# Performance work log

Measured on AMD Instinct MI355X. Metric: run time of the kernel, lower is better.

Reference implementation:

```python
import jax, jax.numpy as jnp
import numpy as np

K_F = 3          # propagation kernel
PAD_F = 1
NUM = K_F * K_F - 1   # 8 non-reference neighbors
IDX_REF = NUM // 2    # 4
PROP_TIME = 18
B, H, W = 4, 240, 1216


def _conv2d_same(x, w, b):
    # x: (B,Cin,H,W), w: (Cout,Cin,kh,kw)
    y = jax.lax.conv_general_dilated(x, w, (1, 1), 'SAME',
                                     dimension_numbers=('NCHW', 'OIHW', 'NCHW'))
    return y + b[None, :, None, None]


def _bilinear(img, y, x):
    # img: (B,H,W); y,x: (B,K,H,W) float sample coords. Zero outside bounds (DCN semantics).
    Bv, Hv, Wv = img.shape
    flat = img.reshape(Bv, -1)
    y0 = jnp.floor(y)
    x0 = jnp.floor(x)
    wy = y - y0
    wx = x - x0

    def g(yy, xx):
        valid = (yy >= 0) & (yy <= Hv - 1) & (xx >= 0) & (xx <= Wv - 1)
        yc = jnp.clip(yy, 0, Hv - 1).astype(jnp.int32)
        xc = jnp.clip(xx, 0, Wv - 1).astype(jnp.int32)
        idx = (yc * Wv + xc).reshape(Bv, -1)
        v = jnp.take_along_axis(flat, idx, axis=1).reshape(yy.shape)
        return jnp.where(valid, v, jnp.zeros((), img.dtype))

    return ((1 - wy) * (1 - wx) * g(y0, x0)
            + (1 - wy) * wx * g(y0, x0 + 1)
            + wy * (1 - wx) * g(y1 := y0 + 1, x0)
            + wy * wx * g(y1, x0 + 1))


def _deform_agg(feat, off, mask, k, pad):
    # Modulated deformable conv with w == 1, b == 0, ch_f == 1.
    # feat: (B,1,H,W); off: (B,K,2,H,W) (dy,dx); mask: (B,K,H,W)
    Bv, _, Hv, Wv = feat.shape
    kk = jnp.arange(k)
    by = (jnp.repeat(kk, k) - pad).astype(feat.dtype)  # kernel base dy, row-major
    bx = (jnp.tile(kk, k) - pad).astype(feat.dtype)    # kernel base dx
    gy = jnp.arange(Hv, dtype=feat.dtype)[None, None, :, None]
    gx = jnp.arange(Wv, dtype=feat.dtype)[None, None, None, :]
    y = gy + by[None, :, None, None] + off[:, :, 0]
    x = gx + bx[None, :, None, None] + off[:, :, 1]
    s = _bilinear(feat[:, 0], y, x)                    # (B,K,H,W)
    return jnp.sum(s * mask, axis=1, keepdims=True)


def setup_inputs() -> dict:
    key = jax.random.key(0)
    k1, k2, k3, k4, k5, k6 = jax.random.split(key, 6)
    feat_init = jax.random.uniform(k1, (B, 1, H, W), jnp.float32)
    guidance = jax.random.normal(k2, (B, 8, H, W), jnp.float32)
    confidence = jax.random.uniform(k3, (B, 1, H, W), jnp.float32)
    dep = jax.random.uniform(k4, (B, 1, H, W), jnp.float32)
    valid = (jax.random.uniform(k5, (B, 1, H, W), jnp.float32) < 0.05)
    feat_fix = dep * valid.astype(jnp.float32)
    w_oa = 0.1 * jax.random.normal(k6, (3 * NUM, 8, 3, 3), jnp.float32)
    b_oa = jnp.zeros((3 * NUM,), jnp.float32)
    aff_scale_const = jnp.full((1,), 0.5 * NUM, jnp.float32)  # gamma * num (TGASS)
    return {'feat_init': feat_init, 'guidance': guidance, 'confidence': confidence,
            'feat_fix': feat_fix, 'w_oa': w_oa, 'b_oa': b_oa,
            'aff_scale_const': aff_scale_const}


def reference(feat_init, guidance, confidence, feat_fix, w_oa, b_oa, aff_scale_const):
    Bv, _, Hv, Wv = guidance.shape
    oa = _conv2d_same(guidance, w_oa, b_oa)                 # (B,24,H,W)
    o1, o2, aff = oa[:, :NUM], oa[:, NUM:2 * NUM], oa[:, 2 * NUM:]
    # torch: cat((o1,o2),1).view(B,num,2,H,W) then insert zero ref offset at idx_ref
    off = jnp.concatenate([o1, o2], axis=1).reshape(Bv, NUM, 2, Hv, Wv)
    zeros = jnp.zeros((Bv, 1, 2, Hv, Wv), off.dtype)
    off = jnp.concatenate([off[:, :IDX_REF], zeros, off[:, IDX_REF:]], axis=1)  # (B,9,2,H,W)

    # TGASS affinity
    aff = jnp.tanh(aff) / (aff_scale_const + 1e-8)          # (B,8,H,W)

    # confidence-weighted affinity: 1x1 deform-sample of confidence at each neighbor offset
    nbr = jnp.array([0, 1, 2, 3, 5, 6, 7, 8])
    off_c = jax.lax.stop_gradient(off[:, nbr])              # (B,8,2,H,W), offsets detached
    gy = jnp.arange(Hv, dtype=aff.dtype)[None, None, :, None]
    gx = jnp.arange(Wv, dtype=aff.dtype)[None, None, None, :]
    conf_aff = _bilinear(confidence[:, 0], gy + off_c[:, :, 0], gx + off_c[:, :, 1])
    aff = aff * conf_aff

    s = jnp.sum(jnp.abs(aff), axis=1, keepdims=True) + 1e-4
    s = jnp.maximum(s, 1.0)                                 # TGASS clamp
    aff = aff / s
    aff_ref = 1.0 - jnp.sum(aff, axis=1, keepdims=True)
    aff9 = jnp.concatenate([aff[:, :IDX_REF], aff_ref, aff[:, IDX_REF:]], axis=1)  # (B,9,H,W)

    # preserve_input mask
    mask_fix = (jnp.sum((feat_fix > 0.0).astype(feat_fix.dtype), axis=1, keepdims=True) > 0.0)
    mask_fix = jax.lax.stop_gradient(mask_fix.astype(feat_fix.dtype))

    def step(feat, _):
        feat = (1.0 - mask_fix) * feat + mask_fix * feat_fix
        feat = _deform_agg(feat, off, aff9, K_F, PAD_F)
        return feat, None

    feat_result, _ = jax.lax.scan(step, feat_init, None, length=PROP_TIME)
    return feat_result, off.reshape(Bv, -1, Hv, Wv), aff9
```

## Files before the change

kernel.cpp:

```cpp
#include <hip/hip_runtime.h>
#include <hip/hip_bf16.h>

#define B_ 4
#define H_ 240
#define W_ 1216
#define HW_ (H_*W_)
#define N1_ (B_*HW_)
#define PT_ 18

#define PR_ 2
#define TROWS2 (PR_ + 10)
#define TCOLS 274

__device__ __forceinline__ bool probe_bf16(const void* scale_ptr) {
    return ((const unsigned short*)scale_ptr)[0] == 0x4080;
}

__device__ __forceinline__ float ldin(const void* p, int i, bool bf) {
    if (bf) {
        unsigned int u = (unsigned int)((const unsigned short*)p)[i];
        return __uint_as_float(u << 16);
    }
    return ((const float*)p)[i];
}

__device__ __forceinline__ void stout(void* p, int i, bool bf, float v) {
    if (bf) ((__hip_bfloat16*)p)[i] = __float2bfloat16(v);
    else    ((float*)p)[i] = v;
}

template<bool BF>
__device__ __forceinline__ float ldT(const void* p, int i) {
    if (BF) {
        unsigned int u = (unsigned int)((const unsigned short*)p)[i];
        return __uint_as_float(u << 16);
    }
    return ((const float*)p)[i];
}

template<bool BF>
__device__ __forceinline__ void stT(void* p, int i, float v) {
    if (BF) ((__hip_bfloat16*)p)[i] = __float2bfloat16(v);
    else    ((float*)p)[i] = v;
}

__global__ __launch_bounds__(256) void k_prep_w(const void* __restrict__ w_oa,
                                                const void* __restrict__ b_oa,
                                                const void* __restrict__ scale,
                                                float* __restrict__ wc) {
    bool bf = probe_bf16(scale);
    int i = blockIdx.x * 256 + threadIdx.x;
    if (i < 1728) wc[i] = ldin(w_oa, i, bf);
    if (i < 24)   wc[1728 + i] = ldin(b_oa, i, bf);
}

__global__ __launch_bounds__(256) void k_init(const void* __restrict__ finit,
                                              const void* __restrict__ ffix,
                                              const void* __restrict__ scale,
                                              float* __restrict__ featA,
                                              float* __restrict__ featB,
                                              unsigned long long* __restrict__ mask64) {
    bool bf = probe_bf16(scale);
    int p = blockIdx.x * 256 + threadIdx.x;
    float fx = ldin(ffix, p, bf);
    float fi = ldin(finit, p, bf);
    bool fixed = fx > 0.0f;
    float v = fixed ? fx : fi;
    featA[p] = v;
    featB[p] = v;
    unsigned long long bal = __ballot(fixed);
    if ((threadIdx.x & 63) == 0) mask64[p >> 6] = bal;
}

__global__ __launch_bounds__(256) void k_conv(const void* __restrict__ guid,
                                              const void* __restrict__ conf,
                                              const void* __restrict__ scale,
                                              const float* __restrict__ wc,
                                              void* __restrict__ d_out,
                                              float* __restrict__ ws_off,
                                              float* __restrict__ ws_aff,
                                              int mode2) {
    bool bf = probe_bf16(scale);
    int p = blockIdx.x * 256 + threadIdx.x;
    if (p >= N1_) return;
    int b = p / HW_;
    int r = p - b * HW_;
    int h = r / W_;
    int w = r - h * W_;

    float g[8][9];
    #pragma unroll
    for (int t = 0; t < 9; ++t) {
        int hh = h + t / 3 - 1;
        int ww = w + t % 3 - 1;
        bool v = (hh >= 0) && (hh < H_) && (ww >= 0) && (ww < W_);
        int idx0 = hh * W_ + ww;
        #pragma unroll
        for (int ci = 0; ci < 8; ++ci)
            g[ci][t] = v ? ldin(guid, (b * 8 + ci) * HW_ + idx0, bf) : 0.0f;
    }

    float oa[24];
    #pragma unroll
    for (int co = 0; co < 24; ++co) {
        float a = wc[1728 + co];
        #pragma unroll
        for (int ci = 0; ci < 8; ++ci)
            #pragma unroll
            for (int t = 0; t < 9; ++t)
                a = fmaf(g[ci][t], wc[(co * 8 + ci) * 9 + t], a);
        oa[co] = a;
    }

    float scl = ldin(scale, 0, bf);
    float inv = 1.0f / (scl + 1e-8f);

    float aft[8];
    int cbase = b * HW_;
    #pragma unroll
    for (int t = 0; t < 8; ++t) {
        float a = tanhf(oa[16 + t]) * inv;
        float y = (float)h + oa[2 * t];
        float x = (float)w + oa[2 * t + 1];
        float y0f = floorf(y), x0f = floorf(x);
        int y0 = (int)y0f, x0 = (int)x0f;
        float wy = y - y0f, wx = x - x0f;
        int y0c = min(max(y0, 0), H_ - 1), y1c = min(max(y0 + 1, 0), H_ - 1);
        int x0c = min(max(x0, 0), W_ - 1), x1c = min(max(x0 + 1, 0), W_ - 1);
        bool vy0 = (y0 >= 0) && (y0 < H_), vy1 = (y0 >= -1) && (y0 < H_ - 1);
        bool vx0 = (x0 >= 0) && (x0 < W_), vx1 = (x0 >= -1) && (x0 < W_ - 1);
        float w00 = (1.0f - wy) * (1.0f - wx); w00 = (vy0 && vx0) ? w00 : 0.0f;
        float w01 = (1.0f - wy) * wx;          w01 = (vy0 && vx1) ? w01 : 0.0f;
        float w10 = wy * (1.0f - wx);          w10 = (vy1 && vx0) ? w10 : 0.0f;
        float w11 = wy * wx;                   w11 = (vy1 && vx1) ? w11 : 0.0f;
        float f00 = ldin(conf, cbase + y0c * W_ + x0c, bf);
        float f01 = ldin(conf, cbase + y0c * W_ + x1c, bf);
        float f10 = ldin(conf, cbase + y1c * W_ + x0c, bf);
        float f11 = ldin(conf, cbase + y1c * W_ + x1c, bf);
        float cv = w00 * f00 + w01 * f01 + w10 * f10 + w11 * f11;
        aft[t] = a * cv;
    }
    float s = 1e-4f;
    #pragma unroll
    for (int t = 0; t < 8; ++t) s += fabsf(aft[t]);
    s = fmaxf(s, 1.0f);
    float rs = 1.0f / s;
    float suma = 0.0f;
    #pragma unroll
    for (int t = 0; t < 8; ++t) { aft[t] *= rs; suma += aft[t]; }
    float aref = 1.0f - suma;

    #pragma unroll
    for (int t = 0; t < 8; ++t) {
        int n9 = t + (t >= 4 ? 1 : 0);
        stout(d_out, N1_ + (b * 18 + 2 * n9)     * HW_ + r, bf, oa[2 * t]);
        stout(d_out, N1_ + (b * 18 + 2 * n9 + 1) * HW_ + r, bf, oa[2 * t + 1]);
        stout(d_out, 19 * N1_ + (b * 9 + n9) * HW_ + r, bf, aft[t]);
    }
    stout(d_out, N1_ + (b * 18 + 8) * HW_ + r, bf, 0.0f);
    stout(d_out, N1_ + (b * 18 + 9) * HW_ + r, bf, 0.0f);
    stout(d_out, 19 * N1_ + (b * 9 + 4) * HW_ + r, bf, aref);

    if (mode2 && bf) {
        #pragma unroll
        for (int t = 0; t < 8; ++t) {
            ws_off[t * N1_ + p]       = oa[2 * t];
            ws_off[(8 + t) * N1_ + p] = oa[2 * t + 1];
            int n9 = t + (t >= 4 ? 1 : 0);
            ws_aff[n9 * N1_ + p] = aft[t];
        }
        ws_aff[4 * N1_ + p] = aref;
    }
}

template<bool BF>
__device__ __forceinline__ void prop_body(float (*tile)[TCOLS],
                                          const float* __restrict__ src,
                                          float* __restrict__ dst,
                                          const float* __restrict__ ws_off,
                                          const float* __restrict__ ws_aff,
                                          const void* __restrict__ d_out_all,
                                          const unsigned long long* __restrict__ mask64,
                                          void* __restrict__ d_out_feat,
                                          int last, int mode2) {
    int tx = threadIdx.x;
    int bx = blockIdx.x;
    int h0 = blockIdx.y * PR_;
    int b  = blockIdx.z;
    int w  = bx * 256 + tx;
    bool active = (w < W_);
    bool use_ws = BF && (mode2 != 0);

    const float* sp = src + b * HW_;
    int row0 = h0 - 5;
    int col0 = bx * 256 - 8;

    for (int idx = tx; idx < TROWS2 * TCOLS; idx += 256) {
        int rr = idx / TCOLS;
        int cc = idx - rr * TCOLS;
        int gy = min(max(row0 + rr, 0), H_ - 1);
        int gx = min(max(col0 + cc, 0), W_ - 1);
        tile[rr][cc] = sp[gy * W_ + gx];
    }
    __syncthreads();
    if (!active) return;

    for (int ry = 0; ry < PR_; ++ry) {
        int h = h0 + ry;
        int r = h * W_ + w;
        int p = b * HW_ + r;

        float oy[8], ox[8], af[9];
        if (use_ws) {
            #pragma unroll
            for (int t = 0; t < 8; ++t) {
                oy[t] = ws_off[t * N1_ + p];
                ox[t] = ws_off[(8 + t) * N1_ + p];
            }
            #pragma unroll
            for (int n = 0; n < 9; ++n) af[n] = ws_aff[n * N1_ + p];
        } else {
            #pragma unroll
            for (int t = 0; t < 8; ++t) {
                int n9 = t + (t >= 4 ? 1 : 0);
                oy[t] = ldT<BF>(d_out_all, N1_ + (b * 18 + 2 * n9)     * HW_ + r);
                ox[t] = ldT<BF>(d_out_all, N1_ + (b * 18 + 2 * n9 + 1) * HW_ + r);
            }
            #pragma unroll
            for (int n = 0; n < 9; ++n)
                af[n] = ldT<BF>(d_out_all, 19 * N1_ + (b * 9 + n) * HW_ + r);
        }

        float acc = af[4] * tile[5 + ry][tx + 8];

        #pragma unroll
        for (int t = 0; t < 8; ++t) {
            int n9 = t + (t >= 4 ? 1 : 0);
            float y = (float)(h + n9 / 3 - 1) + oy[t];
            float x = (float)(w + n9 % 3 - 1) + ox[t];
            float y0f = floorf(y), x0f = floorf(x);
            int y0 = (int)y0f, x0 = (int)x0f;
            float wy = y - y0f, wx = x - x0f;
            int y0c = min(max(y0, 0), H_ - 1), y1c = min(max(y0 + 1, 0), H_ - 1);
            int x0c = min(max(x0, 0), W_ - 1), x1c = min(max(x0 + 1, 0), W_ - 1);
            bool vy0 = (y0 >= 0) && (y0 < H_), vy1 = (y0 >= -1) && (y0 < H_ - 1);
            bool vx0 = (x0 >= 0) && (x0 < W_), vx1 = (x0 >= -1) && (x0 < W_ - 1);
            float w00 = (1.0f - wy) * (1.0f - wx); w00 = (vy0 && vx0) ? w00 : 0.0f;
            float w01 = (1.0f - wy) * wx;          w01 = (vy0 && vx1) ? w01 : 0.0f;
            float w10 = wy * (1.0f - wx);          w10 = (vy1 && vx0) ? w10 : 0.0f;
            float w11 = wy * wx;                   w11 = (vy1 && vx1) ? w11 : 0.0f;

            int sy0 = y0c - row0, sy1 = y1c - row0;
            int sx0 = x0c - col0, sx1 = x1c - col0;
            float f00, f01, f10, f11;
            if ((sy0 >= 0) && (sy1 <= TROWS2 - 1) && (sx0 >= 0) && (sx1 <= TCOLS - 1)) {
                f00 = tile[sy0][sx0];
                f01 = tile[sy0][sx1];
                f10 = tile[sy1][sx0];
                f11 = tile[sy1][sx1];
            } else {
                f00 = sp[y0c * W_ + x0c];
                f01 = sp[y0c * W_ + x1c];
                f10 = sp[y1c * W_ + x0c];
                f11 = sp[y1c * W_ + x1c];
            }
            float v = w00 * f00 + w01 * f01 + w10 * f10 + w11 * f11;
            acc = fmaf(af[n9], v, acc);
        }

        if (last) {
            stT<BF>(d_out_feat, p, acc);
        } else {
            unsigned long long bal = mask64[p >> 6];
            bool fixed = (bal >> (p & 63)) & 1ull;
            if (!fixed) dst[p] = acc;
        }
    }
}

__global__ __launch_bounds__(256) void k_prop(const float* __restrict__ src,
                                              float* __restrict__ dst,
                                              const float* __restrict__ ws_off,
                                              const float* __restrict__ ws_aff,
                                              const void* __restrict__ d_out_all,
                                              const unsigned long long* __restrict__ mask64,
                                              const void* __restrict__ scale,
                                              void* __restrict__ d_out_feat,
                                              int last, int mode2) {
    __shared__ float tile[TROWS2][TCOLS];
    if (probe_bf16(scale))
        prop_body<true>(tile, src, dst, ws_off, ws_aff, d_out_all, mask64,
                        d_out_feat, last, mode2);
    else
        prop_body<false>(tile, src, dst, ws_off, ws_aff, d_out_all, mask64,
                         d_out_feat, last, mode2);
}

extern "C" void kernel_launch(void* const* d_in, const int* in_sizes, int n_in,
                              void* d_out, int out_size, void* d_ws, size_t ws_size,
                              hipStream_t stream) {
    const void* feat_init  = d_in[0];
    const void* guidance   = d_in[1];
    const void* confidence = d_in[2];
    const void* feat_fix   = d_in[3];
    const void* w_oa       = d_in[4];
    const void* b_oa       = d_in[5];
    const void* scale      = d_in[6];

    float* wsf    = (float*)d_ws;
    float* featA  = wsf;
    float* featB  = wsf + N1_;
    float* wc     = wsf + 2 * (size_t)N1_;
    unsigned long long* mask64 =
        (unsigned long long*)(wsf + 2 * (size_t)N1_ + 2048);
    float* ws_off = wsf + 2 * (size_t)N1_ + 2048 + 36480;
    float* ws_aff = ws_off + 16 * (size_t)N1_;

    size_t need2 = ((size_t)27 * N1_ + 2048 + 36480) * sizeof(float);
    int mode2 = (ws_size >= need2) ? 1 : 0;

    int grid = N1_ / 256;
    hipLaunchKernelGGL(k_prep_w, dim3(7), dim3(256), 0, stream, w_oa, b_oa, scale, wc);
    hipLaunchKernelGGL(k_init, dim3(grid), dim3(256), 0, stream,
                       feat_init, feat_fix, scale, featA, featB, mask64);
    hipLaunchKernelGGL(k_conv, dim3(grid), dim3(256), 0, stream,
                       guidance, confidence, scale, wc, d_out, ws_off, ws_aff, mode2);

    float* a = featA;
    float* bbuf = featB;
    dim3 pgrid(5, H_ / PR_, B_);
    for (int it = 0; it < PT_; ++it) {
        int last = (it == PT_ - 1) ? 1 : 0;
        hipLaunchKernelGGL(k_prop, pgrid, dim3(256), 0, stream,
                           a, bbuf, ws_off, ws_aff, d_out, mask64, scale,
                           d_out, last, mode2);
        float* t = a; a = bbuf; bbuf = t;
    }
}
```

Baseline: 955.9 us.

## Pack offsets and affinities into float4 workspace, recompute reference affinity, taller row tiles

The conv kernel now writes the 16 offsets and 8 neighbor affinities as six interleaved float4 arrays, and the fp32 path uses this workspace too instead of reading strided outputs. The propagation kernel reads them with six 16-byte loads instead of 25 scalar loads and recomputes the reference affinity as one minus the sum, which removes one stream. Rows per block go from 2 to 4 so the halo tile is amortized over more rows. The cost is a changed workspace layout, fewer blocks in the grid, and a recomputed reference affinity that may differ slightly in rounding from the stored value.

```diff
diff --git a/kernel.cpp b/kernel.cpp
--- a/kernel.cpp
+++ b/kernel.cpp
@@ -8,7 +8,7 @@
 #define N1_ (B_*HW_)
 #define PT_ 18
 
-#define PR_ 2
+#define PR_ 4
 #define TROWS2 (PR_ + 10)
 #define TCOLS 274
 
@@ -77,8 +77,7 @@
                                               const void* __restrict__ scale,
                                               const float* __restrict__ wc,
                                               void* __restrict__ d_out,
-                                              float* __restrict__ ws_off,
-                                              float* __restrict__ ws_aff,
+                                              float4* __restrict__ pk,
                                               int mode2) {
     bool bf = probe_bf16(scale);
     int p = blockIdx.x * 256 + threadIdx.x;
@@ -161,15 +160,13 @@
     stout(d_out, N1_ + (b * 18 + 9) * HW_ + r, bf, 0.0f);
     stout(d_out, 19 * N1_ + (b * 9 + 4) * HW_ + r, bf, aref);
 
-    if (mode2 && bf) {
-        #pragma unroll
-        for (int t = 0; t < 8; ++t) {
-            ws_off[t * N1_ + p]       = oa[2 * t];
-            ws_off[(8 + t) * N1_ + p] = oa[2 * t + 1];
-            int n9 = t + (t >= 4 ? 1 : 0);
-            ws_aff[n9 * N1_ + p] = aft[t];
-        }
-        ws_aff[4 * N1_ + p] = aref;
+    if (mode2) {
+        pk[0 * (size_t)N1_ + p] = make_float4(oa[0],  oa[1],  oa[2],  oa[3]);
+        pk[1 * (size_t)N1_ + p] = make_float4(oa[4],  oa[5],  oa[6],  oa[7]);
+        pk[2 * (size_t)N1_ + p] = make_float4(oa[8],  oa[9],  oa[10], oa[11]);
+        pk[3 * (size_t)N1_ + p] = make_float4(oa[12], oa[13], oa[14], oa[15]);
+        pk[4 * (size_t)N1_ + p] = make_float4(aft[0], aft[1], aft[2], aft[3]);
+        pk[5 * (size_t)N1_ + p] = make_float4(aft[4], aft[5], aft[6], aft[7]);
     }
 }
 
@@ -177,8 +174,7 @@
 __device__ __forceinline__ void prop_body(float (*tile)[TCOLS],
                                           const float* __restrict__ src,
                                           float* __restrict__ dst,
-                                          const float* __restrict__ ws_off,
-                                          const float* __restrict__ ws_aff,
+                                          const float4* __restrict__ pk,
                                           const void* __restrict__ d_out_all,
                                           const unsigned long long* __restrict__ mask64,
                                           void* __restrict__ d_out_feat,
@@ -189,7 +185,7 @@
     int b  = blockIdx.z;
     int w  = bx * 256 + tx;
     bool active = (w < W_);
-    bool use_ws = BF && (mode2 != 0);
+    bool use_ws = (mode2 != 0);
 
     const float* sp = src + b * HW_;
     int row0 = h0 - 5;
@@ -212,13 +208,21 @@
 
         float oy[8], ox[8], af[9];
         if (use_ws) {
-            #pragma unroll
-            for (int t = 0; t < 8; ++t) {
-                oy[t] = ws_off[t * N1_ + p];
-                ox[t] = ws_off[(8 + t) * N1_ + p];
-            }
-            #pragma unroll
-            for (int n = 0; n < 9; ++n) af[n] = ws_aff[n * N1_ + p];
+            float4 q0 = pk[0 * (size_t)N1_ + p];
+            float4 q1 = pk[1 * (size_t)N1_ + p];
+            float4 q2 = pk[2 * (size_t)N1_ + p];
+            float4 q3 = pk[3 * (size_t)N1_ + p];
+            float4 q4 = pk[4 * (size_t)N1_ + p];
+            float4 q5 = pk[5 * (size_t)N1_ + p];
+            oy[0] = q0.x; ox[0] = q0.y; oy[1] = q0.z; ox[1] = q0.w;
+            oy[2] = q1.x; ox[2] = q1.y; oy[3] = q1.z; ox[3] = q1.w;
+            oy[4] = q2.x; ox[4] = q2.y; oy[5] = q2.z; ox[5] = q2.w;
+            oy[6] = q3.x; ox[6] = q3.y; oy[7] = q3.z; ox[7] = q3.w;
+            af[0] = q4.x; af[1] = q4.y; af[2] = q4.z; af[3] = q4.w;
+            af[5] = q5.x; af[6] = q5.y; af[7] = q5.z; af[8] = q5.w;
+            float suma = q4.x; suma += q4.y; suma += q4.z; suma += q4.w;
+            suma += q5.x; suma += q5.y; suma += q5.z; suma += q5.w;
+            af[4] = 1.0f - suma;
         } else {
             #pragma unroll
             for (int t = 0; t < 8; ++t) {
@@ -280,8 +284,7 @@
 
 __global__ __launch_bounds__(256) void k_prop(const float* __restrict__ src,
                                               float* __restrict__ dst,
-                                              const float* __restrict__ ws_off,
-                                              const float* __restrict__ ws_aff,
+                                              const float4* __restrict__ pk,
                                               const void* __restrict__ d_out_all,
                                               const unsigned long long* __restrict__ mask64,
                                               const void* __restrict__ scale,
@@ -289,10 +292,10 @@
                                               int last, int mode2) {
     __shared__ float tile[TROWS2][TCOLS];
     if (probe_bf16(scale))
-        prop_body<true>(tile, src, dst, ws_off, ws_aff, d_out_all, mask64,
+        prop_body<true>(tile, src, dst, pk, d_out_all, mask64,
                         d_out_feat, last, mode2);
     else
-        prop_body<false>(tile, src, dst, ws_off, ws_aff, d_out_all, mask64,
+        prop_body<false>(tile, src, dst, pk, d_out_all, mask64,
                          d_out_feat, last, mode2);
 }
 
@@ -313,10 +316,9 @@
     float* wc     = wsf + 2 * (size_t)N1_;
     unsigned long long* mask64 =
         (unsigned long long*)(wsf + 2 * (size_t)N1_ + 2048);
-    float* ws_off = wsf + 2 * (size_t)N1_ + 2048 + 36480;
-    float* ws_aff = ws_off + 16 * (size_t)N1_;
-
-    size_t need2 = ((size_t)27 * N1_ + 2048 + 36480) * sizeof(float);
+    float4* pk = (float4*)(wsf + 2 * (size_t)N1_ + 2048 + 36480);
+
+    size_t need2 = ((size_t)26 * N1_ + 2048 + 36480) * sizeof(float);
     int mode2 = (ws_size >= need2) ? 1 : 0;
 
     int grid = N1_ / 256;
@@ -324,7 +326,7 @@
     hipLaunchKernelGGL(k_init, dim3(grid), dim3(256), 0, stream,
                        feat_init, feat_fix, scale, featA, featB, mask64);
     hipLaunchKernelGGL(k_conv, dim3(grid), dim3(256), 0, stream,
-                       guidance, confidence, scale, wc, d_out, ws_off, ws_aff, mode2);
+                       guidance, confidence, scale, wc, d_out, pk, mode2);
 
     float* a = featA;
     float* bbuf = featB;
@@ -332,7 +334,7 @@
     for (int it = 0; it < PT_; ++it) {
         int last = (it == PT_ - 1) ? 1 : 0;
         hipLaunchKernelGGL(k_prop, pgrid, dim3(256), 0, stream,
-                           a, bbuf, ws_off, ws_aff, d_out, mask64, scale,
+                           a, bbuf, pk, d_out, mask64, scale,
                            d_out, last, mode2);
         float* t = a; a = bbuf; bbuf = t;
     }
```

After: 1.188 ms. 1.24x slower.

## Fuse propagation iterations into one cooperative persistent kernel with grid sync

Applied to the files above, without the earlier changes.

Replaces the 18 separate propagation launches with one cooperative kernel. It loops over the iterations, swaps ping-pong buffers and calls grid.sync between steps. Per-pixel offsets and affinities are loaded into registers once instead of being reread from global memory on every iteration, and rows per block go from 2 to 4. The aim is to remove launch overhead and repeated metadata traffic. The risks are higher register pressure, which can lower occupancy or make the co-residency check fail so the old multi-launch path runs, and the cost of grid-wide barriers.

```diff
diff --git a/kernel.cpp b/kernel.cpp
--- a/kernel.cpp
+++ b/kernel.cpp
@@ -1,5 +1,8 @@
 #include <hip/hip_runtime.h>
 #include <hip/hip_bf16.h>
+#include <hip/hip_cooperative_groups.h>
+
+namespace cg = cooperative_groups;
 
 #define B_ 4
 #define H_ 240
@@ -8,7 +11,7 @@
 #define N1_ (B_*HW_)
 #define PT_ 18
 
-#define PR_ 2
+#define PR_ 4
 #define TROWS2 (PR_ + 10)
 #define TCOLS 274
 
@@ -174,6 +177,164 @@
 }
 
 template<bool BF>
+__device__ __forceinline__ float prop_px(const float (*tile)[TCOLS],
+                                         const float* __restrict__ sp,
+                                         const float* oy, const float* ox,
+                                         const float* af,
+                                         int h, int w, int ry,
+                                         int row0, int col0, int tx) {
+    float acc = af[4] * tile[5 + ry][tx + 8];
+    #pragma unroll
+    for (int t = 0; t < 8; ++t) {
+        int n9 = t + (t >= 4 ? 1 : 0);
+        float y = (float)(h + n9 / 3 - 1) + oy[t];
+        float x = (float)(w + n9 % 3 - 1) + ox[t];
+        float y0f = floorf(y), x0f = floorf(x);
+        int y0 = (int)y0f, x0 = (int)x0f;
+        float wy = y - y0f, wx = x - x0f;
+        int y0c = min(max(y0, 0), H_ - 1), y1c = min(max(y0 + 1, 0), H_ - 1);
+        int x0c = min(max(x0, 0), W_ - 1), x1c = min(max(x0 + 1, 0), W_ - 1);
+        bool vy0 = (y0 >= 0) && (y0 < H_), vy1 = (y0 >= -1) && (y0 < H_ - 1);
+        bool vx0 = (x0 >= 0) && (x0 < W_), vx1 = (x0 >= -1) && (x0 < W_ - 1);
+        float w00 = (1.0f - wy) * (1.0f - wx); w00 = (vy0 && vx0) ? w00 : 0.0f;
+        float w01 = (1.0f - wy) * wx;          w01 = (vy0 && vx1) ? w01 : 0.0f;
+        float w10 = wy * (1.0f - wx);          w10 = (vy1 && vx0) ? w10 : 0.0f;
+        float w11 = wy * wx;                   w11 = (vy1 && vx1) ? w11 : 0.0f;
+        int sy0 = y0c - row0, sy1 = y1c - row0;
+        int sx0 = x0c - col0, sx1 = x1c - col0;
+        float f00, f01, f10, f11;
+        if ((sy0 >= 0) && (sy1 <= TROWS2 - 1) && (sx0 >= 0) && (sx1 <= TCOLS - 1)) {
+            f00 = tile[sy0][sx0];
+            f01 = tile[sy0][sx1];
+            f10 = tile[sy1][sx0];
+            f11 = tile[sy1][sx1];
+        } else {
+            f00 = sp[y0c * W_ + x0c];
+            f01 = sp[y0c * W_ + x1c];
+            f10 = sp[y1c * W_ + x0c];
+            f11 = sp[y1c * W_ + x1c];
+        }
+        float v = w00 * f00 + w01 * f01 + w10 * f10 + w11 * f11;
+        acc = fmaf(af[n9], v, acc);
+    }
+    return acc;
+}
+
+template<bool BF>
+__device__ __forceinline__ void load_meta(float* oy, float* ox, float* af,
+                                          const float* __restrict__ ws_off,
+                                          const float* __restrict__ ws_aff,
+                                          const void* __restrict__ d_out_all,
+                                          bool use_ws, int b, int r, int p) {
+    if (use_ws) {
+        #pragma unroll
+        for (int t = 0; t < 8; ++t) {
+            oy[t] = ws_off[t * N1_ + p];
+            ox[t] = ws_off[(8 + t) * N1_ + p];
+        }
+        #pragma unroll
+        for (int n = 0; n < 9; ++n) af[n] = ws_aff[n * N1_ + p];
+    } else {
+        #pragma unroll
+        for (int t = 0; t < 8; ++t) {
+            int n9 = t + (t >= 4 ? 1 : 0);
+            oy[t] = ldT<BF>(d_out_all, N1_ + (b * 18 + 2 * n9)     * HW_ + r);
+            ox[t] = ldT<BF>(d_out_all, N1_ + (b * 18 + 2 * n9 + 1) * HW_ + r);
+        }
+        #pragma unroll
+        for (int n = 0; n < 9; ++n)
+            af[n] = ldT<BF>(d_out_all, 19 * N1_ + (b * 9 + n) * HW_ + r);
+    }
+}
+
+template<bool BF>
+__device__ __forceinline__ void fused_body(float (*tile)[TCOLS],
+                                           float* __restrict__ bufA,
+                                           float* __restrict__ bufB,
+                                           const float* __restrict__ ws_off,
+                                           const float* __restrict__ ws_aff,
+                                           const void* __restrict__ d_out_all,
+                                           const unsigned long long* __restrict__ mask64,
+                                           void* __restrict__ d_out_feat,
+                                           int mode2) {
+    cg::grid_group grid = cg::this_grid();
+    int tx = threadIdx.x;
+    int bx = blockIdx.x;
+    int h0 = blockIdx.y * PR_;
+    int b  = blockIdx.z;
+    int w  = bx * 256 + tx;
+    bool active = (w < W_);
+    bool use_ws = BF && (mode2 != 0);
+    int row0 = h0 - 5;
+    int col0 = bx * 256 - 8;
+
+    float oy[PR_][8], ox[PR_][8], af[PR_][9];
+    if (active) {
+        #pragma unroll
+        for (int ry = 0; ry < PR_; ++ry) {
+            int r = (h0 + ry) * W_ + w;
+            int p = b * HW_ + r;
+            load_meta<BF>(oy[ry], ox[ry], af[ry], ws_off, ws_aff, d_out_all,
+                          use_ws, b, r, p);
+        }
+    }
+
+    const float* src = bufA;
+    float* dst = bufB;
+    for (int it = 0; it < PT_; ++it) {
+        const float* sp = src + b * HW_;
+        for (int idx = tx; idx < TROWS2 * TCOLS; idx += 256) {
+            int rr = idx / TCOLS;
+            int cc = idx - rr * TCOLS;
+            int gy = min(max(row0 + rr, 0), H_ - 1);
+            int gx = min(max(col0 + cc, 0), W_ - 1);
+            tile[rr][cc] = sp[gy * W_ + gx];
+        }
+        __syncthreads();
+
+        if (active) {
+            #pragma unroll
+            for (int ry = 0; ry < PR_; ++ry) {
+                int h = h0 + ry;
+                int r = h * W_ + w;
+                int p = b * HW_ + r;
+                float acc = prop_px<BF>(tile, sp, oy[ry], ox[ry], af[ry],
+                                        h, w, ry, row0, col0, tx);
+                if (it == PT_ - 1) {
+                    stT<BF>(d_out_feat, p, acc);
+                } else {
+                    unsigned long long bal = mask64[p >> 6];
+                    bool fixed = (bal >> (p & 63)) & 1ull;
+                    if (!fixed) dst[p] = acc;
+                }
+            }
+        }
+
+        if (it < PT_ - 1) {
+            const float* t = src; src = dst; dst = (float*)t;
+            grid.sync();
+        }
+    }
+}
+
+__global__ __launch_bounds__(256) void k_prop_fused(float* bufA, float* bufB,
+                                                    const float* ws_off,
+                                                    const float* ws_aff,
+                                                    const void* d_out_all,
+                                                    const unsigned long long* mask64,
+                                                    const void* scale,
+                                                    void* d_out_feat,
+                                                    int mode2) {
+    __shared__ float tile[TROWS2][TCOLS];
+    if (probe_bf16(scale))
+        fused_body<true>(tile, bufA, bufB, ws_off, ws_aff, d_out_all, mask64,
+                         d_out_feat, mode2);
+    else
+        fused_body<false>(tile, bufA, bufB, ws_off, ws_aff, d_out_all, mask64,
+                          d_out_feat, mode2);
+}
+
+template<bool BF>
 __device__ __forceinline__ void prop_body(float (*tile)[TCOLS],
                                           const float* __restrict__ src,
                                           float* __restrict__ dst,
@@ -190,7 +351,6 @@
     int w  = bx * 256 + tx;
     bool active = (w < W_);
     bool use_ws = BF && (mode2 != 0);
-
     const float* sp = src + b * HW_;
     int row0 = h0 - 5;
     int col0 = bx * 256 - 8;
@@ -209,65 +369,9 @@
         int h = h0 + ry;
         int r = h * W_ + w;
         int p = b * HW_ + r;
-
         float oy[8], ox[8], af[9];
-        if (use_ws) {
-            #pragma unroll
-            for (int t = 0; t < 8; ++t) {
-                oy[t] = ws_off[t * N1_ + p];
-                ox[t] = ws_off[(8 + t) * N1_ + p];
-            }
-            #pragma unroll
-            for (int n = 0; n < 9; ++n) af[n] = ws_aff[n * N1_ + p];
-        } else {
-            #pragma unroll
-            for (int t = 0; t < 8; ++t) {
-                int n9 = t + (t >= 4 ? 1 : 0);
-                oy[t] = ldT<BF>(d_out_all, N1_ + (b * 18 + 2 * n9)     * HW_ + r);
-                ox[t] = ldT<BF>(d_out_all, N1_ + (b * 18 + 2 * n9 + 1) * HW_ + r);
-            }
-            #pragma unroll
-            for (int n = 0; n < 9; ++n)
-                af[n] = ldT<BF>(d_out_all, 19 * N1_ + (b * 9 + n) * HW_ + r);
-        }
-
-        float acc = af[4] * tile[5 + ry][tx + 8];
-
-        #pragma unroll
-        for (int t = 0; t < 8; ++t) {
-            int n9 = t + (t >= 4 ? 1 : 0);
-            float y = (float)(h + n9 / 3 - 1) + oy[t];
-            float x = (float)(w + n9 % 3 - 1) + ox[t];
-            float y0f = floorf(y), x0f = floorf(x);
-            int y0 = (int)y0f, x0 = (int)x0f;
-            float wy = y - y0f, wx = x - x0f;
-            int y0c = min(max(y0, 0), H_ - 1), y1c = min(max(y0 + 1, 0), H_ - 1);
-            int x0c = min(max(x0, 0), W_ - 1), x1c = min(max(x0 + 1, 0), W_ - 1);
-            bool vy0 = (y0 >= 0) && (y0 < H_), vy1 = (y0 >= -1) && (y0 < H_ - 1);
-            bool vx0 = (x0 >= 0) && (x0 < W_), vx1 = (x0 >= -1) && (x0 < W_ - 1);
-            float w00 = (1.0f - wy) * (1.0f - wx); w00 = (vy0 && vx0) ? w00 : 0.0f;
-            float w01 = (1.0f - wy) * wx;          w01 = (vy0 && vx1) ? w01 : 0.0f;
-            float w10 = wy * (1.0f - wx);          w10 = (vy1 && vx0) ? w10 : 0.0f;
-            float w11 = wy * wx;                   w11 = (vy1 && vx1) ? w11 : 0.0f;
-
-            int sy0 = y0c - row0, sy1 = y1c - row0;
-            int sx0 = x0c - col0, sx1 = x1c - col0;
-            float f00, f01, f10, f11;
-            if ((sy0 >= 0) && (sy1 <= TROWS2 - 1) && (sx0 >= 0) && (sx1 <= TCOLS - 1)) {
-                f00 = tile[sy0][sx0];
-                f01 = tile[sy0][sx1];
-                f10 = tile[sy1][sx0];
-                f11 = tile[sy1][sx1];
-            } else {
-                f00 = sp[y0c * W_ + x0c];
-                f01 = sp[y0c * W_ + x1c];
-                f10 = sp[y1c * W_ + x0c];
-                f11 = sp[y1c * W_ + x1c];
-            }
-            float v = w00 * f00 + w01 * f01 + w10 * f10 + w11 * f11;
-            acc = fmaf(af[n9], v, acc);
-        }
-
+        load_meta<BF>(oy, ox, af, ws_off, ws_aff, d_out_all, use_ws, b, r, p);
+        float acc = prop_px<BF>(tile, sp, oy, ox, af, h, w, ry, row0, col0, tx);
         if (last) {
             stT<BF>(d_out_feat, p, acc);
         } else {
@@ -326,14 +430,30 @@
     hipLaunchKernelGGL(k_conv, dim3(grid), dim3(256), 0, stream,
                        guidance, confidence, scale, wc, d_out, ws_off, ws_aff, mode2);
 
-    float* a = featA;
-    float* bbuf = featB;
     dim3 pgrid(5, H_ / PR_, B_);
-    for (int it = 0; it < PT_; ++it) {
-        int last = (it == PT_ - 1) ? 1 : 0;
-        hipLaunchKernelGGL(k_prop, pgrid, dim3(256), 0, stream,
-                           a, bbuf, ws_off, ws_aff, d_out, mask64, scale,
-                           d_out, last, mode2);
-        float* t = a; a = bbuf; bbuf = t;
-    }
-}
+    bool fused_ok = false;
+    int maxBlocksPerCU = 0;
+    hipError_t qe = hipOccupancyMaxActiveBlocksPerMultiprocessor(
+        &maxBlocksPerCU, (const void*)k_prop_fused, 256, 0);
+    if (qe == hipSuccess && maxBlocksPerCU * 256 >= (int)(5 * (H_ / PR_) * B_)) {
+        void* args[] = { (void*)&featA, (void*)&featB,
+                         (void*)&ws_off, (void*)&ws_aff,
+                         (void*)&d_out, (void*)&mask64,
+                         (void*)&scale, (void*)&d_out, (void*)&mode2 };
+        hipError_t le = hipLaunchCooperativeKernel(
+            (const void*)k_prop_fused, pgrid, dim3(256), args, 0, stream);
+        fused_ok = (le == hipSuccess);
+    }
+
+    if (!fused_ok) {
+        float* a = featA;
+        float* bbuf = featB;
+        for (int it = 0; it < PT_; ++it) {
+            int last = (it == PT_ - 1) ? 1 : 0;
+            hipLaunchKernelGGL(k_prop, pgrid, dim3(256), 0, stream,
+                               a, bbuf, ws_off, ws_aff, d_out, mask64, scale,
+                               d_out, last, mode2);
+            float* t = a; a = bbuf; bbuf = t;
+        }
+    }
+}
```

Measured after the change: 946.2 us. About the same (-1.0%).
